# Optimization experiments

Measured on AMD Instinct MI355X. Metric: run time of the kernel, lower is better.

The kernel has to match this reference:

```python
import jax, jax.numpy as jnp
import numpy as np

N = 20000; E = 120000; D = 1024; H = 8; C = D // H; L = 2; EPS = 1e-5


def setup_inputs() -> dict:
    key = jax.random.key(0)
    ks = jax.random.split(key, 12)
    s = 0.03  # init scale (glorot-ish for d=1024)
    return {
        'x': jax.random.normal(ks[0], (N, D), jnp.float32),
        'edge_index': jax.random.randint(ks[1], (2, E), 0, N),
        'edge_attr': jax.random.randint(ks[2], (E,), 0, 5),
        'node_types': jax.random.randint(ks[3], (N,), 0, 6),
        'node_type_emb': jax.random.normal(ks[4], (6, D), jnp.float32) * s,
        'edge_type_emb': jax.random.normal(ks[5], (5, D), jnp.float32) * s,
        'W_l': jax.random.normal(ks[6], (L, D, D), jnp.float32) * s,
        'b_l': jnp.zeros((L, D), jnp.float32),
        'W_r': jax.random.normal(ks[7], (L, D, D), jnp.float32) * s,
        'b_r': jnp.zeros((L, D), jnp.float32),
        'W_e': jax.random.normal(ks[8], (L, D, D), jnp.float32) * s,
        'att': jax.random.normal(ks[9], (L, H, C), jnp.float32) * s,
        'bias': jnp.zeros((L, D), jnp.float32),
        'ln_gamma': jnp.ones((L, D), jnp.float32),
        'ln_beta': jnp.zeros((L, D), jnp.float32),
        'W_out': jax.random.normal(ks[10], (D, D), jnp.float32) * s,
        'b_out': jnp.zeros((D,), jnp.float32),
        'gate': jnp.array([0.5], jnp.float32),
    }


def _layer_norm(y, g, b):
    mu = y.mean(-1, keepdims=True)
    var = ((y - mu) ** 2).mean(-1, keepdims=True)
    return (y - mu) * jax.lax.rsqrt(var + EPS) * g + b


def reference(x, edge_index, edge_attr, node_types, node_type_emb, edge_type_emb,
              W_l, b_l, W_r, b_r, W_e, att, bias, ln_gamma, ln_beta,
              W_out, b_out, gate):
    src, dst = edge_index[0], edge_index[1]
    e_emb = edge_type_emb[edge_attr]                       # [E, D]
    # PyG add_self_loops(fill_value='mean'): self-loop edge attr = mean of
    # incoming edge attrs (0 if no incoming edges)
    deg = jax.ops.segment_sum(jnp.ones((E,), x.dtype), dst, num_segments=N)
    loop_e = jax.ops.segment_sum(e_emb, dst, num_segments=N) / jnp.maximum(deg, 1.0)[:, None]
    idx = jnp.arange(N, dtype=src.dtype)
    src_a = jnp.concatenate([src, idx])                    # [E+N]
    dst_a = jnp.concatenate([dst, idx])
    e_all = jnp.concatenate([e_emb, loop_e], axis=0)       # [E+N, D]

    h = x + node_type_emb[node_types]
    for l in range(L):
        xl = (h @ W_l[l] + b_l[l]).reshape(N, H, C)        # lin_l (source)
        xr = (h @ W_r[l] + b_r[l]).reshape(N, H, C)        # lin_r (target)
        ee = (e_all @ W_e[l]).reshape(-1, H, C)            # lin_edge (no bias)
        s = jax.nn.leaky_relu(xl[src_a] + xr[dst_a] + ee, 0.2)
        logits = jnp.einsum('ehc,hc->eh', s, att[l])       # [E+N, H]
        # segment softmax over incoming edges per target node
        mx = jax.ops.segment_max(logits, dst_a, num_segments=N)
        ex = jnp.exp(logits - mx[dst_a])
        den = jax.ops.segment_sum(ex, dst_a, num_segments=N)
        alpha = ex / den[dst_a]                            # [E+N, H]
        out = jax.ops.segment_sum(xl[src_a] * alpha[..., None], dst_a,
                                  num_segments=N).reshape(N, D) + bias[l]
        h2 = jax.nn.elu(out)                               # dropout is identity in eval
        h = _layer_norm(h2 + h, ln_gamma[l], ln_beta[l])
    return x + gate * (h @ W_out + b_out)
```

## Files before the change

kernel.cpp:

```cpp
#include <hip/hip_runtime.h>


#define NN 20000
#define NE 120000
#define DD 1024
#define NH 8

typedef __attribute__((ext_vector_type(4))) float f32x4;
typedef __bf16 bf16x8 __attribute__((ext_vector_type(8)));

__device__ __forceinline__ unsigned short f2bf(float f) {
  unsigned int u = __float_as_uint(f);
  u += 0x7FFFu + ((u >> 16) & 1u);
  return (unsigned short)(u >> 16);
}
__device__ __forceinline__ float bf2f(unsigned short u) {
  return __uint_as_float((unsigned int)u << 16);
}
__device__ __forceinline__ void unpack8(uint4 u, float* f) {
  f[0] = __uint_as_float(u.x << 16); f[1] = __uint_as_float(u.x & 0xFFFF0000u);
  f[2] = __uint_as_float(u.y << 16); f[3] = __uint_as_float(u.y & 0xFFFF0000u);
  f[4] = __uint_as_float(u.z << 16); f[5] = __uint_as_float(u.z & 0xFFFF0000u);
  f[6] = __uint_as_float(u.w << 16); f[7] = __uint_as_float(u.w & 0xFFFF0000u);
}


__global__ __launch_bounds__(256) void count_kernel(
    const int* __restrict__ EI, const int* __restrict__ eattr, int* __restrict__ cnt) {
  int e = blockIdx.x * 256 + threadIdx.x;
  if (e < NE) {
    int d = EI[NE + e];
    int t = eattr[e];
    atomicAdd(&cnt[d * 5 + t], 1);
  }
}

__global__ __launch_bounds__(1024) void scan_kernel(
    const int* __restrict__ cnt, int* __restrict__ rowptr, int* __restrict__ cursor) {
  __shared__ int wsum[16];
  __shared__ int carry_s;
  int tid = threadIdx.x, lane = tid & 63, wv = tid >> 6;
  if (tid == 0) carry_s = 0;
  __syncthreads();
  for (int base = 0; base < NN; base += 1024) {
    int n = base + tid;
    int d = 0;
    if (n < NN) {
      const int* c = cnt + n * 5;
      d = c[0] + c[1] + c[2] + c[3] + c[4];
    }
    int v = d;
    #pragma unroll
    for (int off = 1; off < 64; off <<= 1) {
      int t = __shfl_up(v, off);
      if (lane >= off) v += t;
    }
    if (lane == 63) wsum[wv] = v;
    __syncthreads();
    int woff = 0;
    #pragma unroll
    for (int w = 0; w < 16; ++w) if (w < wv) woff += wsum[w];
    int carry = carry_s;
    int excl = carry + woff + v - d;
    if (n < NN) { rowptr[n] = excl; cursor[n] = excl; }
    __syncthreads();
    if (tid == 0) {
      int t = 0;
      #pragma unroll
      for (int w = 0; w < 16; ++w) t += wsum[w];
      carry_s = carry + t;
    }
    __syncthreads();
  }
  if (tid == 0) rowptr[NN] = carry_s;
}

__global__ __launch_bounds__(256) void scatter_kernel(
    const int* __restrict__ EI, const int* __restrict__ eattr,
    int* __restrict__ cursor, int* __restrict__ epk) {
  int e = blockIdx.x * 256 + threadIdx.x;
  if (e < NE) {
    int d = EI[NE + e];
    int s = EI[e];
    int t = eattr[e];
    int pos = atomicAdd(&cursor[d], 1);
    epk[pos] = (s << 3) | t;
  }
}


__global__ __launch_bounds__(256) void init_h_kernel(
    const float* __restrict__ x, const int* __restrict__ ntypes,
    const float* __restrict__ ntemb, float* __restrict__ h,
    unsigned short* __restrict__ hb) {
  int idx = blockIdx.x * 256 + threadIdx.x;
  int n = idx >> 8;
  int d4 = idx & 255;
  int t = ntypes[n];
  float4 xv = ((const float4*)x)[idx];
  float4 ev = ((const float4*)ntemb)[t * 256 + d4];
  float4 o;
  o.x = xv.x + ev.x; o.y = xv.y + ev.y; o.z = xv.z + ev.z; o.w = xv.w + ev.w;
  ((float4*)h)[idx] = o;
  ushort4 hv;
  hv.x = f2bf(o.x); hv.y = f2bf(o.y); hv.z = f2bf(o.z); hv.w = f2bf(o.w);
  ((ushort4*)hb)[idx] = hv;
}


__global__ __launch_bounds__(256) void transpose_w_kernel(
    const float* __restrict__ W, unsigned short* __restrict__ WT) {
  __shared__ float tile[32][33];
  int tx = threadIdx.x & 31, ty = threadIdx.x >> 5;
  int bx = blockIdx.x * 32;
  int by = blockIdx.y * 32;
  #pragma unroll
  for (int r = 0; r < 4; ++r)
    tile[ty + r * 8][tx] = W[(size_t)(by + ty + r * 8) * DD + bx + tx];
  __syncthreads();
  #pragma unroll
  for (int r = 0; r < 4; ++r)
    WT[(size_t)(bx + ty + r * 8) * DD + by + tx] = f2bf(tile[tx][ty + r * 8]);
}


__global__ __launch_bounds__(256) void m_kernel(
    const float* __restrict__ ete, const float* __restrict__ We, float* __restrict__ M) {
  __shared__ float red[4][5][64];
  const int jl = threadIdx.x & 63;
  const int kc = threadIdx.x >> 6;
  const int j = blockIdx.x * 64 + jl;
  float acc[5] = {0.f, 0.f, 0.f, 0.f, 0.f};
  const int k0 = kc * 256;
  for (int k = k0; k < k0 + 256; ++k) {
    float w = We[(size_t)k * DD + j];
    #pragma unroll
    for (int t = 0; t < 5; ++t) acc[t] += ete[t * DD + k] * w;
  }
  #pragma unroll
  for (int t = 0; t < 5; ++t) red[kc][t][jl] = acc[t];
  __syncthreads();
  if (threadIdx.x < 64) {
    #pragma unroll
    for (int t = 0; t < 5; ++t)
      M[t * DD + blockIdx.x * 64 + threadIdx.x] =
          red[0][t][threadIdx.x] + red[1][t][threadIdx.x] +
          red[2][t][threadIdx.x] + red[3][t][threadIdx.x];
  }
}


__global__ __launch_bounds__(256) void gemm_bf16(
    const unsigned short* __restrict__ A, const unsigned short* __restrict__ BT,
    const float* __restrict__ bias0, const float* __restrict__ bias1,
    void* __restrict__ C0v, void* __restrict__ C1v,
    const float* __restrict__ resid, const float* __restrict__ gatep,
    int M, int mode) {
  __shared__ unsigned short lsA[128 * 32];
  __shared__ unsigned short lsB[128 * 32];
  const int tid = threadIdx.x;
  const int lane = tid & 63;
  const int wv = tid >> 6;
  const int wm = wv & 1, wn = wv >> 1;

  const int nwg = gridDim.x * gridDim.y;
  const int lid = blockIdx.y * gridDim.x + blockIdx.x;
  const int cpx = nwg >> 3;
  const int swz = (lid & 7) * cpx + (lid >> 3);
  const int bm = swz / gridDim.x, bn = swz % gridDim.x;

  const int row0 = bm * 128, col0 = bn * 128;
  const int l15 = lane & 15, quad = lane >> 4;

  f32x4 acc[4][4];
  #pragma unroll
  for (int mt = 0; mt < 4; ++mt)
    #pragma unroll
    for (int nt = 0; nt < 4; ++nt) {
      f32x4 z = {0.f, 0.f, 0.f, 0.f};
      acc[mt][nt] = z;
    }

  const int r_in = lane >> 2;
  const int kchunk = (lane & 3) * 8;

  for (int kk = 0; kk < DD; kk += 32) {
    #pragma unroll
    for (int j = 0; j < 2; ++j) {
      int r = wv * 32 + j * 16;
      int gr = row0 + r + r_in;
      if (gr > M - 1) gr = M - 1;
      const unsigned short* gpA = A + (size_t)gr * DD + kk + kchunk;
      __builtin_amdgcn_global_load_lds(
          (const __attribute__((address_space(1))) unsigned int*)gpA,
          (__attribute__((address_space(3))) unsigned int*)(lsA + r * 32), 16, 0, 0);
      const unsigned short* gpB = BT + (size_t)(col0 + r + r_in) * DD + kk + kchunk;
      __builtin_amdgcn_global_load_lds(
          (const __attribute__((address_space(1))) unsigned int*)gpB,
          (__attribute__((address_space(3))) unsigned int*)(lsB + r * 32), 16, 0, 0);
    }
    __syncthreads();
    bf16x8 af[4], bfr[4];
    #pragma unroll
    for (int mt = 0; mt < 4; ++mt)
      af[mt] = *(const bf16x8*)(lsA + (wm * 64 + mt * 16 + l15) * 32 + quad * 8);
    #pragma unroll
    for (int nt = 0; nt < 4; ++nt)
      bfr[nt] = *(const bf16x8*)(lsB + (wn * 64 + nt * 16 + l15) * 32 + quad * 8);
    #pragma unroll
    for (int mt = 0; mt < 4; ++mt)
      #pragma unroll
      for (int nt = 0; nt < 4; ++nt)
        acc[mt][nt] = __builtin_amdgcn_mfma_f32_16x16x32_bf16(af[mt], bfr[nt], acc[mt][nt], 0, 0, 0);
    __syncthreads();
  }

  if (mode == 0) {
    unsigned short* Cb = (unsigned short*)(bn < 8 ? C0v : C1v);
    const float* bp = (bn < 8) ? bias0 : bias1;
    int coff = (bn < 8) ? 0 : 1024;
    #pragma unroll
    for (int mt = 0; mt < 4; ++mt) {
      #pragma unroll
      for (int r = 0; r < 4; ++r) {
        int grow = row0 + wm * 64 + mt * 16 + quad * 4 + r;
        if (grow >= M) continue;
        #pragma unroll
        for (int nt = 0; nt < 4; ++nt) {
          int c = col0 - coff + wn * 64 + nt * 16 + l15;
          Cb[(size_t)grow * DD + c] = f2bf(acc[mt][nt][r] + bp[c]);
        }
      }
    }
  } else {
    float* Cp = (float*)C0v;
    float g = gatep[0];
    #pragma unroll
    for (int mt = 0; mt < 4; ++mt) {
      #pragma unroll
      for (int r = 0; r < 4; ++r) {
        int grow = row0 + wm * 64 + mt * 16 + quad * 4 + r;
        if (grow >= M) continue;
        #pragma unroll
        for (int nt = 0; nt < 4; ++nt) {
          int c = col0 + wn * 64 + nt * 16 + l15;
          float v = acc[mt][nt][r] + bias0[c];
          Cp[(size_t)grow * DD + c] = resid[(size_t)grow * DD + c] + g * v;
        }
      }
    }
  }
}


__global__ __launch_bounds__(256) void attn_kernel(
    const unsigned short* __restrict__ xlb, const unsigned short* __restrict__ xrb,
    const int* __restrict__ rowptr, const int* __restrict__ epk,
    const int* __restrict__ cnt, const float* __restrict__ Mbuf,
    const float* __restrict__ attl, const float* __restrict__ biasl,
    const float* __restrict__ gammal, const float* __restrict__ betal,
    float* __restrict__ h, unsigned short* __restrict__ hb, int write_h) {
  const int lane = threadIdx.x & 63;
  const int wv = threadIdx.x >> 6;
  const int n = blockIdx.x * 4 + wv;
  if (n >= NN) return;
  const int ch = lane * 16;

  const int beg = rowptr[n], end = rowptr[n + 1];
  const int* c5 = cnt + n * 5;
  int c0 = c5[0], c1 = c5[1], c2 = c5[2], c3 = c5[3], c4 = c5[4];

  float xrf[16], attf[16];
  {
    const uint4* xp = (const uint4*)(xrb + (size_t)n * DD + ch);
    uint4 a = xp[0], b = xp[1];
    unpack8(a, xrf); unpack8(b, xrf + 8);
    const float4* ap = (const float4*)(attl + ch);
    #pragma unroll
    for (int q = 0; q < 4; ++q) {
      float4 t = ap[q];
      attf[q * 4 + 0] = t.x; attf[q * 4 + 1] = t.y;
      attf[q * 4 + 2] = t.z; attf[q * 4 + 3] = t.w;
    }
  }
  float acc[16];
  #pragma unroll
  for (int c = 0; c < 16; ++c) acc[c] = 0.f;
  float den = 0.f;

  for (int base = beg; base < end; base += 64) {
    int cc = min(64, end - base);
    int packed = 0;
    if (lane < cc) packed = epk[base + lane];
    for (int j = 0; j < cc; ++j) {
      int pk = __shfl(packed, j);
      int src = pk >> 3, at = pk & 7;
      const uint4* vp = (const uint4*)(xlb + (size_t)src * DD + ch);
      uint4 v0 = vp[0], v1 = vp[1];
      const float4* mp = (const float4*)(Mbuf + at * DD + ch);
      float vf[16];
      unpack8(v0, vf); unpack8(v1, vf + 8);
      float lg = 0.f;
      #pragma unroll
      for (int q = 0; q < 4; ++q) {
        float4 m = mp[q];
        float s0 = vf[q * 4 + 0] + xrf[q * 4 + 0] + m.x; s0 = fmaxf(s0, 0.2f * s0);
        float s1 = vf[q * 4 + 1] + xrf[q * 4 + 1] + m.y; s1 = fmaxf(s1, 0.2f * s1);
        float s2 = vf[q * 4 + 2] + xrf[q * 4 + 2] + m.z; s2 = fmaxf(s2, 0.2f * s2);
        float s3 = vf[q * 4 + 3] + xrf[q * 4 + 3] + m.w; s3 = fmaxf(s3, 0.2f * s3);
        lg += s0 * attf[q * 4 + 0] + s1 * attf[q * 4 + 1]
            + s2 * attf[q * 4 + 2] + s3 * attf[q * 4 + 3];
      }
      lg += __shfl_xor(lg, 1);
      lg += __shfl_xor(lg, 2);
      lg += __shfl_xor(lg, 4);
      float p = __expf(lg);
      den += p;
      #pragma unroll
      for (int c = 0; c < 16; ++c) acc[c] += p * vf[c];
    }
  }

  {
    float inv = 1.f / fmaxf((float)(c0 + c1 + c2 + c3 + c4), 1.f);
    float w0 = c0 * inv, w1 = c1 * inv, w2 = c2 * inv, w3 = c3 * inv, w4 = c4 * inv;
    const uint4* vp = (const uint4*)(xlb + (size_t)n * DD + ch);
    uint4 v0 = vp[0], v1 = vp[1];
    float vf[16];
    unpack8(v0, vf); unpack8(v1, vf + 8);
    const float* m0 = Mbuf + 0 * DD + ch;
    const float* m1 = Mbuf + 1 * DD + ch;
    const float* m2 = Mbuf + 2 * DD + ch;
    const float* m3 = Mbuf + 3 * DD + ch;
    const float* m4 = Mbuf + 4 * DD + ch;
    float lg = 0.f;
    #pragma unroll
    for (int c = 0; c < 16; ++c) {
      float ee = w0 * m0[c] + w1 * m1[c] + w2 * m2[c] + w3 * m3[c] + w4 * m4[c];
      float s = vf[c] + xrf[c] + ee;
      s = fmaxf(s, 0.2f * s);
      lg += s * attf[c];
    }
    lg += __shfl_xor(lg, 1);
    lg += __shfl_xor(lg, 2);
    lg += __shfl_xor(lg, 4);
    float p = __expf(lg);
    den += p;
    #pragma unroll
    for (int c = 0; c < 16; ++c) acc[c] += p * vf[c];
  }

  float invd = 1.f / den;
  float y[16];
  float s1 = 0.f, s2 = 0.f;
  {
    const float4* bp = (const float4*)(biasl + ch);
    const float4* hp = (const float4*)(h + (size_t)n * DD + ch);
    #pragma unroll
    for (int q = 0; q < 4; ++q) {
      float4 b4 = bp[q];
      float4 h4 = hp[q];
      float o0 = acc[q * 4 + 0] * invd + b4.x;
      float o1 = acc[q * 4 + 1] * invd + b4.y;
      float o2 = acc[q * 4 + 2] * invd + b4.z;
      float o3 = acc[q * 4 + 3] * invd + b4.w;
      o0 = o0 > 0.f ? o0 : (__expf(o0) - 1.f);
      o1 = o1 > 0.f ? o1 : (__expf(o1) - 1.f);
      o2 = o2 > 0.f ? o2 : (__expf(o2) - 1.f);
      o3 = o3 > 0.f ? o3 : (__expf(o3) - 1.f);
      y[q * 4 + 0] = o0 + h4.x; y[q * 4 + 1] = o1 + h4.y;
      y[q * 4 + 2] = o2 + h4.z; y[q * 4 + 3] = o3 + h4.w;
      s1 += y[q * 4 + 0] + y[q * 4 + 1] + y[q * 4 + 2] + y[q * 4 + 3];
      s2 += y[q * 4 + 0] * y[q * 4 + 0] + y[q * 4 + 1] * y[q * 4 + 1]
          + y[q * 4 + 2] * y[q * 4 + 2] + y[q * 4 + 3] * y[q * 4 + 3];
    }
  }
  #pragma unroll
  for (int off = 1; off < 64; off <<= 1) {
    s1 += __shfl_xor(s1, off);
    s2 += __shfl_xor(s2, off);
  }
  float mu = s1 * (1.f / 1024.f);
  float var = s2 * (1.f / 1024.f) - mu * mu;
  float rs = rsqrtf(var + 1e-5f);
  {
    const float4* gp = (const float4*)(gammal + ch);
    const float4* bp = (const float4*)(betal + ch);
    float4* hp = (float4*)(h + (size_t)n * DD + ch);
    uint4* hbp = (uint4*)(hb + (size_t)n * DD + ch);
    uint4 pk0, pk1;
    unsigned int* pk = (unsigned int*)&pk0;
    #pragma unroll
    for (int q = 0; q < 4; ++q) {
      float4 g4 = gp[q];
      float4 b4 = bp[q];
      float4 o4;
      o4.x = (y[q * 4 + 0] - mu) * rs * g4.x + b4.x;
      o4.y = (y[q * 4 + 1] - mu) * rs * g4.y + b4.y;
      o4.z = (y[q * 4 + 2] - mu) * rs * g4.z + b4.z;
      o4.w = (y[q * 4 + 3] - mu) * rs * g4.w + b4.w;
      if (write_h) hp[q] = o4;
      unsigned int lo = (unsigned int)f2bf(o4.x) | ((unsigned int)f2bf(o4.y) << 16);
      unsigned int hi = (unsigned int)f2bf(o4.z) | ((unsigned int)f2bf(o4.w) << 16);
      if (q < 2) { pk[q * 2] = lo; pk[q * 2 + 1] = hi; }
      else {
        unsigned int* pkh = (unsigned int*)&pk1;
        pkh[(q - 2) * 2] = lo; pkh[(q - 2) * 2 + 1] = hi;
      }
    }
    hbp[0] = pk0;
    hbp[1] = pk1;
  }
}


extern "C" void kernel_launch(void* const* d_in, const int* in_sizes, int n_in,
                              void* d_out, int out_size, void* d_ws, size_t ws_size,
                              hipStream_t stream) {
  (void)in_sizes; (void)n_in; (void)out_size; (void)ws_size;
  const float* x      = (const float*)d_in[0];
  const int*   EI     = (const int*)d_in[1];
  const int*   eattr  = (const int*)d_in[2];
  const int*   ntypes = (const int*)d_in[3];
  const float* ntemb  = (const float*)d_in[4];
  const float* etemb  = (const float*)d_in[5];
  const float* W_l    = (const float*)d_in[6];
  const float* b_l    = (const float*)d_in[7];
  const float* W_r    = (const float*)d_in[8];
  const float* b_r    = (const float*)d_in[9];
  const float* W_e    = (const float*)d_in[10];
  const float* att    = (const float*)d_in[11];
  const float* bias   = (const float*)d_in[12];
  const float* gamma  = (const float*)d_in[13];
  const float* beta   = (const float*)d_in[14];
  const float* W_out  = (const float*)d_in[15];
  const float* b_out  = (const float*)d_in[16];
  const float* gate   = (const float*)d_in[17];
  float* out = (float*)d_out;

  char* ws = (char*)d_ws;
  size_t off = 0;
  auto alloc = [&](size_t bytes) {
    char* p = ws + off;
    off = (off + bytes + 255) & ~(size_t)255;
    return p;
  };
  float*          h       = (float*)alloc((size_t)NN * DD * 4);
  unsigned short* hb      = (unsigned short*)alloc((size_t)NN * DD * 2);
  unsigned short* xlb     = (unsigned short*)alloc((size_t)NN * DD * 2);
  unsigned short* xrb     = (unsigned short*)alloc((size_t)NN * DD * 2);
  unsigned short* WTcat   = (unsigned short*)alloc((size_t)2 * DD * DD * 2);
  unsigned short* WT2     = (unsigned short*)alloc((size_t)DD * DD * 2);
  float*          Mbuf    = (float*)alloc((size_t)5 * DD * 4);
  int*            countb  = (int*)alloc((size_t)NN * 5 * 4);
  int*            rowptr  = (int*)alloc((size_t)(NN + 1) * 4);
  int*            cursor  = (int*)alloc((size_t)NN * 4);
  int*            epk     = (int*)alloc((size_t)NE * 4);

  hipMemsetAsync(countb, 0, (size_t)NN * 5 * 4, stream);
  count_kernel<<<(NE + 255) / 256, 256, 0, stream>>>(EI, eattr, countb);
  scan_kernel<<<1, 1024, 0, stream>>>(countb, rowptr, cursor);
  scatter_kernel<<<(NE + 255) / 256, 256, 0, stream>>>(EI, eattr, cursor, epk);
  init_h_kernel<<<NN, 256, 0, stream>>>(x, ntypes, ntemb, h, hb);

  dim3 tgrid(DD / 32, DD / 32);
  dim3 ggrid2(16, (NN + 127) / 128);
  dim3 ggrid1(8, (NN + 127) / 128);
  for (int l = 0; l < 2; ++l) {
    transpose_w_kernel<<<tgrid, 256, 0, stream>>>(W_l + (size_t)l * DD * DD, WTcat);
    transpose_w_kernel<<<tgrid, 256, 0, stream>>>(W_r + (size_t)l * DD * DD, WTcat + (size_t)DD * DD);
    m_kernel<<<DD / 64, 256, 0, stream>>>(etemb, W_e + (size_t)l * DD * DD, Mbuf);
    gemm_bf16<<<ggrid2, 256, 0, stream>>>(hb, WTcat, b_l + l * DD, b_r + l * DD,
                                          xlb, xrb, nullptr, nullptr, NN, 0);
    attn_kernel<<<(NN + 3) / 4, 256, 0, stream>>>(xlb, xrb, rowptr, epk, countb, Mbuf,
                                                  att + l * DD, bias + l * DD,
                                                  gamma + l * DD, beta + l * DD, h, hb,
                                                  l == 0 ? 1 : 0);
  }
  transpose_w_kernel<<<tgrid, 256, 0, stream>>>(W_out, WT2);
  gemm_bf16<<<ggrid1, 256, 0, stream>>>(hb, WT2, b_out, nullptr,
                                        out, nullptr, x, gate, NN, 1);
}
```

Baseline: 877.8 us.

## Assign one block per node in attention kernel instead of one wave per node

The attention/aggregation kernel now uses a whole 256-thread block per destination node, with each lane handling 4 channels instead of 16. Per-head logit reduction widens to 32 lanes, and the LayerNorm statistics are combined across the four waves through shared memory and a block barrier. The goal is more parallelism and memory-level concurrency per node and lower register pressure on the gather loop. The cost is 4x more blocks, each doing the edge loop and index shuffles redundantly per wave, smaller per-lane loads, and an added __syncthreads.

```diff
diff --git a/kernel.cpp b/kernel.cpp
--- a/kernel.cpp
+++ b/kernel.cpp
@@ -22,6 +22,10 @@
   f[2] = __uint_as_float(u.y << 16); f[3] = __uint_as_float(u.y & 0xFFFF0000u);
   f[4] = __uint_as_float(u.z << 16); f[5] = __uint_as_float(u.z & 0xFFFF0000u);
   f[6] = __uint_as_float(u.w << 16); f[7] = __uint_as_float(u.w & 0xFFFF0000u);
+}
+__device__ __forceinline__ void unpack4(uint2 u, float* f) {
+  f[0] = __uint_as_float(u.x << 16); f[1] = __uint_as_float(u.x & 0xFFFF0000u);
+  f[2] = __uint_as_float(u.y << 16); f[3] = __uint_as_float(u.y & 0xFFFF0000u);
 }
 
 
@@ -260,32 +264,24 @@
     const float* __restrict__ attl, const float* __restrict__ biasl,
     const float* __restrict__ gammal, const float* __restrict__ betal,
     float* __restrict__ h, unsigned short* __restrict__ hb, int write_h) {
+  __shared__ float red1[4], red2[4];
   const int lane = threadIdx.x & 63;
   const int wv = threadIdx.x >> 6;
-  const int n = blockIdx.x * 4 + wv;
-  if (n >= NN) return;
-  const int ch = lane * 16;
+  const int n = blockIdx.x;
+  const int ch = wv * 256 + lane * 4;
 
   const int beg = rowptr[n], end = rowptr[n + 1];
   const int* c5 = cnt + n * 5;
   int c0 = c5[0], c1 = c5[1], c2 = c5[2], c3 = c5[3], c4 = c5[4];
 
-  float xrf[16], attf[16];
+  float xrf[4], attf[4];
   {
-    const uint4* xp = (const uint4*)(xrb + (size_t)n * DD + ch);
-    uint4 a = xp[0], b = xp[1];
-    unpack8(a, xrf); unpack8(b, xrf + 8);
-    const float4* ap = (const float4*)(attl + ch);
-    #pragma unroll
-    for (int q = 0; q < 4; ++q) {
-      float4 t = ap[q];
-      attf[q * 4 + 0] = t.x; attf[q * 4 + 1] = t.y;
-      attf[q * 4 + 2] = t.z; attf[q * 4 + 3] = t.w;
-    }
-  }
-  float acc[16];
-  #pragma unroll
-  for (int c = 0; c < 16; ++c) acc[c] = 0.f;
+    uint2 a = *(const uint2*)(xrb + (size_t)n * DD + ch);
+    unpack4(a, xrf);
+    float4 t = *(const float4*)(attl + ch);
+    attf[0] = t.x; attf[1] = t.y; attf[2] = t.z; attf[3] = t.w;
+  }
+  float acc0 = 0.f, acc1 = 0.f, acc2 = 0.f, acc3 = 0.f;
   float den = 0.f;
 
   for (int base = beg; base < end; base += 64) {
@@ -295,121 +291,99 @@
     for (int j = 0; j < cc; ++j) {
       int pk = __shfl(packed, j);
       int src = pk >> 3, at = pk & 7;
-      const uint4* vp = (const uint4*)(xlb + (size_t)src * DD + ch);
-      uint4 v0 = vp[0], v1 = vp[1];
-      const float4* mp = (const float4*)(Mbuf + at * DD + ch);
-      float vf[16];
-      unpack8(v0, vf); unpack8(v1, vf + 8);
-      float lg = 0.f;
-      #pragma unroll
-      for (int q = 0; q < 4; ++q) {
-        float4 m = mp[q];
-        float s0 = vf[q * 4 + 0] + xrf[q * 4 + 0] + m.x; s0 = fmaxf(s0, 0.2f * s0);
-        float s1 = vf[q * 4 + 1] + xrf[q * 4 + 1] + m.y; s1 = fmaxf(s1, 0.2f * s1);
-        float s2 = vf[q * 4 + 2] + xrf[q * 4 + 2] + m.z; s2 = fmaxf(s2, 0.2f * s2);
-        float s3 = vf[q * 4 + 3] + xrf[q * 4 + 3] + m.w; s3 = fmaxf(s3, 0.2f * s3);
-        lg += s0 * attf[q * 4 + 0] + s1 * attf[q * 4 + 1]
-            + s2 * attf[q * 4 + 2] + s3 * attf[q * 4 + 3];
-      }
+      uint2 v = *(const uint2*)(xlb + (size_t)src * DD + ch);
+      float4 m = *(const float4*)(Mbuf + at * DD + ch);
+      float vf[4];
+      unpack4(v, vf);
+      float s0 = vf[0] + xrf[0] + m.x; s0 = fmaxf(s0, 0.2f * s0);
+      float s1 = vf[1] + xrf[1] + m.y; s1 = fmaxf(s1, 0.2f * s1);
+      float s2 = vf[2] + xrf[2] + m.z; s2 = fmaxf(s2, 0.2f * s2);
+      float s3 = vf[3] + xrf[3] + m.w; s3 = fmaxf(s3, 0.2f * s3);
+      float lg = s0 * attf[0] + s1 * attf[1] + s2 * attf[2] + s3 * attf[3];
       lg += __shfl_xor(lg, 1);
       lg += __shfl_xor(lg, 2);
       lg += __shfl_xor(lg, 4);
+      lg += __shfl_xor(lg, 8);
+      lg += __shfl_xor(lg, 16);
       float p = __expf(lg);
       den += p;
-      #pragma unroll
-      for (int c = 0; c < 16; ++c) acc[c] += p * vf[c];
+      acc0 += p * vf[0]; acc1 += p * vf[1];
+      acc2 += p * vf[2]; acc3 += p * vf[3];
     }
   }
 
   {
     float inv = 1.f / fmaxf((float)(c0 + c1 + c2 + c3 + c4), 1.f);
     float w0 = c0 * inv, w1 = c1 * inv, w2 = c2 * inv, w3 = c3 * inv, w4 = c4 * inv;
-    const uint4* vp = (const uint4*)(xlb + (size_t)n * DD + ch);
-    uint4 v0 = vp[0], v1 = vp[1];
-    float vf[16];
-    unpack8(v0, vf); unpack8(v1, vf + 8);
-    const float* m0 = Mbuf + 0 * DD + ch;
-    const float* m1 = Mbuf + 1 * DD + ch;
-    const float* m2 = Mbuf + 2 * DD + ch;
-    const float* m3 = Mbuf + 3 * DD + ch;
-    const float* m4 = Mbuf + 4 * DD + ch;
-    float lg = 0.f;
-    #pragma unroll
-    for (int c = 0; c < 16; ++c) {
-      float ee = w0 * m0[c] + w1 * m1[c] + w2 * m2[c] + w3 * m3[c] + w4 * m4[c];
-      float s = vf[c] + xrf[c] + ee;
-      s = fmaxf(s, 0.2f * s);
-      lg += s * attf[c];
-    }
+    uint2 v = *(const uint2*)(xlb + (size_t)n * DD + ch);
+    float vf[4];
+    unpack4(v, vf);
+    float4 m0 = *(const float4*)(Mbuf + 0 * DD + ch);
+    float4 m1 = *(const float4*)(Mbuf + 1 * DD + ch);
+    float4 m2 = *(const float4*)(Mbuf + 2 * DD + ch);
+    float4 m3 = *(const float4*)(Mbuf + 3 * DD + ch);
+    float4 m4 = *(const float4*)(Mbuf + 4 * DD + ch);
+    float e0 = w0 * m0.x + w1 * m1.x + w2 * m2.x + w3 * m3.x + w4 * m4.x;
+    float e1 = w0 * m0.y + w1 * m1.y + w2 * m2.y + w3 * m3.y + w4 * m4.y;
+    float e2 = w0 * m0.z + w1 * m1.z + w2 * m2.z + w3 * m3.z + w4 * m4.z;
+    float e3 = w0 * m0.w + w1 * m1.w + w2 * m2.w + w3 * m3.w + w4 * m4.w;
+    float s0 = vf[0] + xrf[0] + e0; s0 = fmaxf(s0, 0.2f * s0);
+    float s1 = vf[1] + xrf[1] + e1; s1 = fmaxf(s1, 0.2f * s1);
+    float s2 = vf[2] + xrf[2] + e2; s2 = fmaxf(s2, 0.2f * s2);
+    float s3 = vf[3] + xrf[3] + e3; s3 = fmaxf(s3, 0.2f * s3);
+    float lg = s0 * attf[0] + s1 * attf[1] + s2 * attf[2] + s3 * attf[3];
     lg += __shfl_xor(lg, 1);
     lg += __shfl_xor(lg, 2);
     lg += __shfl_xor(lg, 4);
+    lg += __shfl_xor(lg, 8);
+    lg += __shfl_xor(lg, 16);
     float p = __expf(lg);
     den += p;
-    #pragma unroll
-    for (int c = 0; c < 16; ++c) acc[c] += p * vf[c];
+    acc0 += p * vf[0]; acc1 += p * vf[1];
+    acc2 += p * vf[2]; acc3 += p * vf[3];
   }
 
   float invd = 1.f / den;
-  float y[16];
-  float s1 = 0.f, s2 = 0.f;
-  {
-    const float4* bp = (const float4*)(biasl + ch);
-    const float4* hp = (const float4*)(h + (size_t)n * DD + ch);
-    #pragma unroll
-    for (int q = 0; q < 4; ++q) {
-      float4 b4 = bp[q];
-      float4 h4 = hp[q];
-      float o0 = acc[q * 4 + 0] * invd + b4.x;
-      float o1 = acc[q * 4 + 1] * invd + b4.y;
-      float o2 = acc[q * 4 + 2] * invd + b4.z;
-      float o3 = acc[q * 4 + 3] * invd + b4.w;
-      o0 = o0 > 0.f ? o0 : (__expf(o0) - 1.f);
-      o1 = o1 > 0.f ? o1 : (__expf(o1) - 1.f);
-      o2 = o2 > 0.f ? o2 : (__expf(o2) - 1.f);
-      o3 = o3 > 0.f ? o3 : (__expf(o3) - 1.f);
-      y[q * 4 + 0] = o0 + h4.x; y[q * 4 + 1] = o1 + h4.y;
-      y[q * 4 + 2] = o2 + h4.z; y[q * 4 + 3] = o3 + h4.w;
-      s1 += y[q * 4 + 0] + y[q * 4 + 1] + y[q * 4 + 2] + y[q * 4 + 3];
-      s2 += y[q * 4 + 0] * y[q * 4 + 0] + y[q * 4 + 1] * y[q * 4 + 1]
-          + y[q * 4 + 2] * y[q * 4 + 2] + y[q * 4 + 3] * y[q * 4 + 3];
-    }
-  }
+  float4 b4 = *(const float4*)(biasl + ch);
+  float4 h4 = *(const float4*)(h + (size_t)n * DD + ch);
+  float o0 = acc0 * invd + b4.x;
+  float o1 = acc1 * invd + b4.y;
+  float o2 = acc2 * invd + b4.z;
+  float o3 = acc3 * invd + b4.w;
+  o0 = o0 > 0.f ? o0 : (__expf(o0) - 1.f);
+  o1 = o1 > 0.f ? o1 : (__expf(o1) - 1.f);
+  o2 = o2 > 0.f ? o2 : (__expf(o2) - 1.f);
+  o3 = o3 > 0.f ? o3 : (__expf(o3) - 1.f);
+  float y0 = o0 + h4.x, y1 = o1 + h4.y, y2 = o2 + h4.z, y3 = o3 + h4.w;
+  float s1r = y0 + y1 + y2 + y3;
+  float s2r = y0 * y0 + y1 * y1 + y2 * y2 + y3 * y3;
   #pragma unroll
   for (int off = 1; off < 64; off <<= 1) {
-    s1 += __shfl_xor(s1, off);
-    s2 += __shfl_xor(s2, off);
-  }
-  float mu = s1 * (1.f / 1024.f);
-  float var = s2 * (1.f / 1024.f) - mu * mu;
+    s1r += __shfl_xor(s1r, off);
+    s2r += __shfl_xor(s2r, off);
+  }
+  if (lane == 0) { red1[wv] = s1r; red2[wv] = s2r; }
+  __syncthreads();
+  float t1 = red1[0] + red1[1] + red1[2] + red1[3];
+  float t2 = red2[0] + red2[1] + red2[2] + red2[3];
+  float mu = t1 * (1.f / 1024.f);
+  float var = t2 * (1.f / 1024.f) - mu * mu;
   float rs = rsqrtf(var + 1e-5f);
   {
-    const float4* gp = (const float4*)(gammal + ch);
-    const float4* bp = (const float4*)(betal + ch);
-    float4* hp = (float4*)(h + (size_t)n * DD + ch);
-    uint4* hbp = (uint4*)(hb + (size_t)n * DD + ch);
-    uint4 pk0, pk1;
-    unsigned int* pk = (unsigned int*)&pk0;
-    #pragma unroll
-    for (int q = 0; q < 4; ++q) {
-      float4 g4 = gp[q];
-      float4 b4 = bp[q];
-      float4 o4;
-      o4.x = (y[q * 4 + 0] - mu) * rs * g4.x + b4.x;
-      o4.y = (y[q * 4 + 1] - mu) * rs * g4.y + b4.y;
-      o4.z = (y[q * 4 + 2] - mu) * rs * g4.z + b4.z;
-      o4.w = (y[q * 4 + 3] - mu) * rs * g4.w + b4.w;
-      if (write_h) hp[q] = o4;
-      unsigned int lo = (unsigned int)f2bf(o4.x) | ((unsigned int)f2bf(o4.y) << 16);
-      unsigned int hi = (unsigned int)f2bf(o4.z) | ((unsigned int)f2bf(o4.w) << 16);
-      if (q < 2) { pk[q * 2] = lo; pk[q * 2 + 1] = hi; }
-      else {
-        unsigned int* pkh = (unsigned int*)&pk1;
-        pkh[(q - 2) * 2] = lo; pkh[(q - 2) * 2 + 1] = hi;
-      }
-    }
-    hbp[0] = pk0;
-    hbp[1] = pk1;
+    float4 g4 = *(const float4*)(gammal + ch);
+    float4 be4 = *(const float4*)(betal + ch);
+    float w0 = (y0 - mu) * rs * g4.x + be4.x;
+    float w1 = (y1 - mu) * rs * g4.y + be4.y;
+    float w2 = (y2 - mu) * rs * g4.z + be4.z;
+    float w3 = (y3 - mu) * rs * g4.w + be4.w;
+    if (write_h) {
+      float4 o4; o4.x = w0; o4.y = w1; o4.z = w2; o4.w = w3;
+      *(float4*)(h + (size_t)n * DD + ch) = o4;
+    }
+    uint2 pk;
+    pk.x = (unsigned int)f2bf(w0) | ((unsigned int)f2bf(w1) << 16);
+    pk.y = (unsigned int)f2bf(w2) | ((unsigned int)f2bf(w3) << 16);
+    *(uint2*)(hb + (size_t)n * DD + ch) = pk;
   }
 }
 
@@ -472,10 +446,10 @@
     m_kernel<<<DD / 64, 256, 0, stream>>>(etemb, W_e + (size_t)l * DD * DD, Mbuf);
     gemm_bf16<<<ggrid2, 256, 0, stream>>>(hb, WTcat, b_l + l * DD, b_r + l * DD,
                                           xlb, xrb, nullptr, nullptr, NN, 0);
-    attn_kernel<<<(NN + 3) / 4, 256, 0, stream>>>(xlb, xrb, rowptr, epk, countb, Mbuf,
-                                                  att + l * DD, bias + l * DD,
-                                                  gamma + l * DD, beta + l * DD, h, hb,
-                                                  l == 0 ? 1 : 0);
+    attn_kernel<<<NN, 256, 0, stream>>>(xlb, xrb, rowptr, epk, countb, Mbuf,
+                                        att + l * DD, bias + l * DD,
+                                        gamma + l * DD, beta + l * DD, h, hb,
+                                        l == 0 ? 1 : 0);
   }
   transpose_w_kernel<<<tgrid, 256, 0, stream>>>(W_out, WT2);
   gemm_bf16<<<ggrid1, 256, 0, stream>>>(hb, WT2, b_out, nullptr,
```

New measurement: 809.8 us. -7.8%, faster.
